# Performance work log

Hardware: AMD Instinct MI355X
Metric: run time of the kernel (lower is better)

The kernel has to match this reference:

```python
import jax, jax.numpy as jnp
import numpy as np

S, B, I, H, O = 1024, 64, 512, 2048, 512


def setup_inputs() -> dict:
    key = jax.random.key(0)
    k1, k2, k3, k4, k5 = jax.random.split(key, 5)
    X = jax.random.normal(k1, (S, B, I), dtype=jnp.float32)
    W_ih = jax.random.normal(k2, (H, I), dtype=jnp.float32) * (1.0 / np.sqrt(I))
    hh = jax.random.uniform(k3, (H,), dtype=jnp.float32)  # clamped-to-[-1,1] diagonal recurrence
    W_ho = jax.random.normal(k4, (O, H), dtype=jnp.float32) * (1.0 / np.sqrt(H))
    b_ho = jax.random.normal(k5, (O,), dtype=jnp.float32) * 0.01
    return {"X": X, "W_ih": W_ih, "hh": hh, "W_ho": W_ho, "b_ho": b_ho}


def reference(X, W_ih, hh, W_ho, b_ho):
    # Batch the input->hidden projection over the whole sequence in one GEMM:
    # u[s,b,h] = X[s,b,i] @ W_ih[h,i]^T
    u = jnp.einsum('sbi,hi->sbh', X, W_ih)
    h0 = jnp.zeros((X.shape[1], W_ih.shape[0]), dtype=X.dtype)

    def step(h, u_t):
        h_new = jnp.abs(u_t + hh * h)
        return h_new, None

    h_final, _ = jax.lax.scan(step, h0, u)
    Y = h_final @ W_ho.T + b_ho  # [B, O]
    return Y
```

## Files before the change

kernel.cpp:

```cpp
#include <hip/hip_runtime.h>
#include <hip/hip_bf16.h>
#include <stdint.h>

#define S_LEN 1024
#define B_SZ  64
#define I_SZ  512
#define H_SZ  2048
#define O_SZ  512
#define BH    (B_SZ * H_SZ)

typedef __bf16  bf16x8 __attribute__((ext_vector_type(8)));
typedef float   f32x4  __attribute__((ext_vector_type(4)));

static __device__ __forceinline__ ushort f2bf(float f) {
  union { float f; unsigned u; } v; v.f = f;
  unsigned r = v.u + 0x7FFFu + ((v.u >> 16) & 1u);
  return (ushort)(r >> 16);
}
static __device__ __forceinline__ float bf2f(ushort u) {
  return __builtin_bit_cast(float, (unsigned)u << 16);
}

#define GLOAD_LDS16(gp, lp) \
  __builtin_amdgcn_global_load_lds( \
      (__attribute__((address_space(1))) void*)(gp), \
      (__attribute__((address_space(3))) void*)(lp), 16, 0, 0)

__global__ __launch_bounds__(256) void convert_f32_bf16_kernel(
    const float4* __restrict__ in, ushort4* __restrict__ out, int n4) {
  int i = blockIdx.x * 256 + threadIdx.x;
  if (i >= n4) return;
  float4 v = in[i];
  ushort4 o; o.x = f2bf(v.x); o.y = f2bf(v.y); o.z = f2bf(v.z); o.w = f2bf(v.w);
  out[i] = o;
}

__global__ __launch_bounds__(256, 3) void fused_gemm_scan_kernel(
    const float* __restrict__ X,
    const ushort* __restrict__ Wbf,
    const float* __restrict__ hh,
    float* __restrict__ hstate) {
  __shared__ __align__(16) ushort smem[17408];
  ushort* As = smem;
  ushort* Bs = smem + 9216;
  ushort* Cs = smem;

  const int tid  = threadIdx.x;
  const int wave = tid >> 6;
  const int lane = tid & 63;

  const int bid = blockIdx.x;
  const int x = bid & 7;
  const int g = bid >> 3;
  const int b  = (x << 3) | (g & 7);
  const int ht = g >> 3;

  const int wm = (wave >> 1) * 64;
  const int wn = (wave & 1) * 64;
  const int ml = lane & 15;
  const int q  = lane >> 4;

  const int arow0 = wave * 32 + (lane >> 3);
  const size_t offA = (size_t)arow0 * (B_SZ * I_SZ) + (size_t)b * I_SZ + (lane & 7) * 8;

  const int r0     = wave * 32;
  const int srow   = lane >> 3;
  const int schunk = ((lane & 7) - srow) & 7;
  const ushort* gB = Wbf + (size_t)(ht * 128 + r0 + srow) * I_SZ + schunk * 8;
  ushort* lB = Bs + r0 * 64;

  int aoff[2], boff[2];
  aoff[0] = q * 8;
  aoff[1] = (4 + q) * 8;
  boff[0] = ((q + ml) & 7) * 8;
  boff[1] = ((4 + q + ml) & 7) * 8;
  int arow[4], brow[4];
  #pragma unroll
  for (int i = 0; i < 4; ++i) {
    arow[i] = (wm + i * 16 + ml) * 72;
    brow[i] = (wn + i * 16 + ml) * 64;
  }

  float c = 0.0f, p = 0.0f;
  if (tid < 128) c = hh[ht * 128 + tid];

  float4 ar[8];
  {
    const float* gp = X + offA;
    #pragma unroll
    for (int j = 0; j < 4; ++j) {
      ar[2 * j]     = *(const float4*)(gp + (size_t)j * (8 * B_SZ * I_SZ));
      ar[2 * j + 1] = *(const float4*)(gp + (size_t)j * (8 * B_SZ * I_SZ) + 4);
    }
  }

  for (int st = 0; st < 8; ++st) {
    f32x4 acc[4][4] = {};

    for (int kt = 0; kt < I_SZ / 64; ++kt) {
      __syncthreads();
      #pragma unroll
      for (int j = 0; j < 4; ++j) {
        union { __bf16 h[8]; uint4 v; } uvt;
        uvt.h[0] = (__bf16)ar[2 * j].x;     uvt.h[1] = (__bf16)ar[2 * j].y;
        uvt.h[2] = (__bf16)ar[2 * j].z;     uvt.h[3] = (__bf16)ar[2 * j].w;
        uvt.h[4] = (__bf16)ar[2 * j + 1].x; uvt.h[5] = (__bf16)ar[2 * j + 1].y;
        uvt.h[6] = (__bf16)ar[2 * j + 1].z; uvt.h[7] = (__bf16)ar[2 * j + 1].w;
        *(uint4*)&As[(arow0 + j * 8) * 72 + (lane & 7) * 8] = uvt.v;
      }
      #pragma unroll
      for (int jj = 0; jj < 4; ++jj)
        GLOAD_LDS16(gB + (size_t)(jj * 8) * I_SZ + kt * 64, lB + jj * 512);
      {
        int nst = (kt == 7) ? st + 1 : st;
        int nkt = (kt == 7) ? 0 : kt + 1;
        if (nst < 8) {
          const float* gp = X + offA + (size_t)nst * (128 * B_SZ * I_SZ) + nkt * 64;
          #pragma unroll
          for (int j = 0; j < 4; ++j) {
            ar[2 * j]     = *(const float4*)(gp + (size_t)j * (8 * B_SZ * I_SZ));
            ar[2 * j + 1] = *(const float4*)(gp + (size_t)j * (8 * B_SZ * I_SZ) + 4);
          }
        }
      }
      __syncthreads();
      #pragma unroll
      for (int ks = 0; ks < 2; ++ks) {
        bf16x8 af[4], bfr[4];
        #pragma unroll
        for (int i = 0; i < 4; ++i) {
          af[i]  = *(const bf16x8*)&As[arow[i] + (ks * 4) * 8 + aoff[0] - q * 8 + q * 8];
          bfr[i] = *(const bf16x8*)&Bs[brow[i] + boff[ks]];
        }
        #pragma unroll
        for (int i = 0; i < 4; ++i)
          af[i] = *(const bf16x8*)&As[arow[i] + (ks * 4 + q) * 8];
        #pragma unroll
        for (int mi = 0; mi < 4; ++mi)
          #pragma unroll
          for (int ni = 0; ni < 4; ++ni)
            acc[mi][ni] = __builtin_amdgcn_mfma_f32_16x16x32_bf16(
                af[mi], bfr[ni], acc[mi][ni], 0, 0, 0);
      }
    }

    __syncthreads();
    const int sb = wm + q * 4;
    #pragma unroll
    for (int mi = 0; mi < 4; ++mi) {
      #pragma unroll
      for (int ni = 0; ni < 4; ++ni) {
        ushort4 o;
        o.x = f2bf(acc[mi][ni][0]); o.y = f2bf(acc[mi][ni][1]);
        o.z = f2bf(acc[mi][ni][2]); o.w = f2bf(acc[mi][ni][3]);
        *(ushort4*)&Cs[(wn + ni * 16 + ml) * 132 + sb + mi * 16] = o;
      }
    }
    __syncthreads();

    if (tid < 128) {
      const ushort* col = &Cs[tid * 132];
      #pragma unroll
      for (int s0 = 0; s0 < 128; s0 += 16) {
        ushort4 v0 = *(const ushort4*)&col[s0];
        ushort4 v1 = *(const ushort4*)&col[s0 + 4];
        ushort4 v2 = *(const ushort4*)&col[s0 + 8];
        ushort4 v3 = *(const ushort4*)&col[s0 + 12];
        p = fmaf(c, fabsf(p), bf2f(v0.x)); p = fmaf(c, fabsf(p), bf2f(v0.y));
        p = fmaf(c, fabsf(p), bf2f(v0.z)); p = fmaf(c, fabsf(p), bf2f(v0.w));
        p = fmaf(c, fabsf(p), bf2f(v1.x)); p = fmaf(c, fabsf(p), bf2f(v1.y));
        p = fmaf(c, fabsf(p), bf2f(v1.z)); p = fmaf(c, fabsf(p), bf2f(v1.w));
        p = fmaf(c, fabsf(p), bf2f(v2.x)); p = fmaf(c, fabsf(p), bf2f(v2.y));
        p = fmaf(c, fabsf(p), bf2f(v2.z)); p = fmaf(c, fabsf(p), bf2f(v2.w));
        p = fmaf(c, fabsf(p), bf2f(v3.x)); p = fmaf(c, fabsf(p), bf2f(v3.y));
        p = fmaf(c, fabsf(p), bf2f(v3.z)); p = fmaf(c, fabsf(p), bf2f(v3.w));
      }
    }
  }

  if (tid < 128) hstate[(size_t)b * H_SZ + ht * 128 + tid] = fabsf(p);
}

__global__ __launch_bounds__(256) void init_y_kernel(
    const float* __restrict__ bho, float* __restrict__ Y) {
  int idx = blockIdx.x * 256 + threadIdx.x;
  Y[idx] = bho[idx & (O_SZ - 1)];
}

__global__ __launch_bounds__(256) void final_tiled_kernel(
    const float* __restrict__ hstate, const float* __restrict__ Who,
    float* __restrict__ Y) {
  __shared__ float Ws[64 * 68];
  __shared__ float Hs[64 * 68];
  const int tid = threadIdx.x;
  const int og = blockIdx.x, kc = blockIdx.y;
  const int to = tid & 15, tb = tid >> 4;
  float acc[4][4] = {};
  #pragma unroll
  for (int ks = 0; ks < 2; ++ks) {
    const int k0 = kc * 128 + ks * 64;
    const int r = tid >> 2, cg = (tid & 3) * 16;
    #pragma unroll
    for (int i2 = 0; i2 < 4; ++i2) {
      *(float4*)&Ws[r * 68 + cg + i2 * 4] =
          *(const float4*)&Who[(size_t)(og * 64 + r) * H_SZ + k0 + cg + i2 * 4];
      *(float4*)&Hs[r * 68 + cg + i2 * 4] =
          *(const float4*)&hstate[(size_t)r * H_SZ + k0 + cg + i2 * 4];
    }
    __syncthreads();
    #pragma unroll 4
    for (int k = 0; k < 64; ++k) {
      float wv[4], hv[4];
      #pragma unroll
      for (int jj2 = 0; jj2 < 4; ++jj2) wv[jj2] = Ws[(to * 4 + jj2) * 68 + k];
      #pragma unroll
      for (int ii = 0; ii < 4; ++ii) hv[ii] = Hs[(tb * 4 + ii) * 68 + k];
      #pragma unroll
      for (int ii = 0; ii < 4; ++ii)
        #pragma unroll
        for (int jj2 = 0; jj2 < 4; ++jj2)
          acc[ii][jj2] += hv[ii] * wv[jj2];
    }
    __syncthreads();
  }
  #pragma unroll
  for (int ii = 0; ii < 4; ++ii)
    #pragma unroll
    for (int jj2 = 0; jj2 < 4; ++jj2)
      atomicAdd(&Y[(size_t)(tb * 4 + ii) * O_SZ + og * 64 + to * 4 + jj2],
                acc[ii][jj2]);
}

extern "C" void kernel_launch(void* const* d_in, const int* in_sizes, int n_in,
                              void* d_out, int out_size, void* d_ws, size_t ws_size,
                              hipStream_t stream) {
  (void)in_sizes; (void)n_in; (void)out_size; (void)ws_size;
  const float* X   = (const float*)d_in[0];
  const float* Wih = (const float*)d_in[1];
  const float* hh  = (const float*)d_in[2];
  const float* Who = (const float*)d_in[3];
  const float* bho = (const float*)d_in[4];
  float* Y = (float*)d_out;

  const size_t WBF = (size_t)H_SZ * I_SZ * 2;

  char* w = (char*)d_ws;
  ushort* Wbf    = (ushort*)w;
  float*  hstate = (float*) (w + WBF);

  {
    int n4w = (int)((size_t)H_SZ * I_SZ / 4);
    convert_f32_bf16_kernel<<<n4w / 256, 256, 0, stream>>>(
        (const float4*)Wih, (ushort4*)Wbf, n4w);
  }

  fused_gemm_scan_kernel<<<1024, 256, 0, stream>>>(X, Wbf, hh, hstate);

  init_y_kernel<<<(B_SZ * O_SZ) / 256, 256, 0, stream>>>(bho, Y);
  final_tiled_kernel<<<dim3(O_SZ / 64, 16), 256, 0, stream>>>(hstate, Who, Y);
}
```

Measured before the change: 387.6 us.

## Software-pipeline fused GEMM-scan, overlap scan with next tile, fuse output projection

Restructures the fused GEMM+scan kernel into a single flattened loop over 64 k-steps. Global-to-LDS loads for the next step and the A conversion for the step after are issued before the current MFMAs, with explicit waitcnt and barrier control. The result tile now has its own LDS region, so the scan of the previous 128-step chunk runs in the same iterations as the next chunk's GEMM instead of serialising after it. The output projection is folded into the kernel's epilogue using atomics, removing the hstate round trip and the separate final kernel. The cost is doubled LDS, occupancy dropping from 3 to 2 blocks, and redundant Who reads across blocks.

Result: slower. 418.1 us (+7.9%).

```diff
diff --git a/kernel.cpp b/kernel.cpp
--- a/kernel.cpp
+++ b/kernel.cpp
@@ -7,7 +7,6 @@
 #define I_SZ  512
 #define H_SZ  2048
 #define O_SZ  512
-#define BH    (B_SZ * H_SZ)
 
 typedef __bf16  bf16x8 __attribute__((ext_vector_type(8)));
 typedef float   f32x4  __attribute__((ext_vector_type(4)));
@@ -35,25 +34,67 @@
   out[i] = o;
 }
 
-__global__ __launch_bounds__(256, 3) void fused_gemm_scan_kernel(
+__global__ __launch_bounds__(256) void init_y_kernel(
+    const float* __restrict__ bho, float* __restrict__ Y) {
+  int idx = blockIdx.x * 256 + threadIdx.x;
+  Y[idx] = bho[idx & (O_SZ - 1)];
+}
+
+#define CVT_WRITE_A() do { \
+    _Pragma("unroll") \
+    for (int j_ = 0; j_ < 4; ++j_) { \
+      union { __bf16 h[8]; uint4 v; } uvt_; \
+      uvt_.h[0] = (__bf16)ar[2*j_].x;   uvt_.h[1] = (__bf16)ar[2*j_].y; \
+      uvt_.h[2] = (__bf16)ar[2*j_].z;   uvt_.h[3] = (__bf16)ar[2*j_].w; \
+      uvt_.h[4] = (__bf16)ar[2*j_+1].x; uvt_.h[5] = (__bf16)ar[2*j_+1].y; \
+      uvt_.h[6] = (__bf16)ar[2*j_+1].z; uvt_.h[7] = (__bf16)ar[2*j_+1].w; \
+      *(uint4*)&As[(arow0 + j_ * 8) * 72 + (lane & 7) * 8] = uvt_.v; \
+    } } while (0)
+
+#define PREFETCH_A(T) do { \
+    const float* gp_ = X + offA + (size_t)((T) >> 3) * (128 * B_SZ * I_SZ) \
+                         + (size_t)(((T) & 7) * 64); \
+    _Pragma("unroll") \
+    for (int j_ = 0; j_ < 4; ++j_) { \
+      ar[2*j_]   = *(const float4*)(gp_ + (size_t)j_ * (8 * B_SZ * I_SZ)); \
+      ar[2*j_+1] = *(const float4*)(gp_ + (size_t)j_ * (8 * B_SZ * I_SZ) + 4); \
+    } } while (0)
+
+#define SCAN16(colp, s0_) do { \
+    ushort4 v0 = *(const ushort4*)&(colp)[(s0_)]; \
+    ushort4 v1 = *(const ushort4*)&(colp)[(s0_) + 4]; \
+    ushort4 v2 = *(const ushort4*)&(colp)[(s0_) + 8]; \
+    ushort4 v3 = *(const ushort4*)&(colp)[(s0_) + 12]; \
+    p = fmaf(c, fabsf(p), bf2f(v0.x)); p = fmaf(c, fabsf(p), bf2f(v0.y)); \
+    p = fmaf(c, fabsf(p), bf2f(v0.z)); p = fmaf(c, fabsf(p), bf2f(v0.w)); \
+    p = fmaf(c, fabsf(p), bf2f(v1.x)); p = fmaf(c, fabsf(p), bf2f(v1.y)); \
+    p = fmaf(c, fabsf(p), bf2f(v1.z)); p = fmaf(c, fabsf(p), bf2f(v1.w)); \
+    p = fmaf(c, fabsf(p), bf2f(v2.x)); p = fmaf(c, fabsf(p), bf2f(v2.y)); \
+    p = fmaf(c, fabsf(p), bf2f(v2.z)); p = fmaf(c, fabsf(p), bf2f(v2.w)); \
+    p = fmaf(c, fabsf(p), bf2f(v3.x)); p = fmaf(c, fabsf(p), bf2f(v3.y)); \
+    p = fmaf(c, fabsf(p), bf2f(v3.z)); p = fmaf(c, fabsf(p), bf2f(v3.w)); \
+  } while (0)
+
+__global__ __launch_bounds__(256, 2) void fused_gemm_scan_kernel(
     const float* __restrict__ X,
     const ushort* __restrict__ Wbf,
     const float* __restrict__ hh,
-    float* __restrict__ hstate) {
-  __shared__ __align__(16) ushort smem[17408];
+    const float* __restrict__ Who,
+    float* __restrict__ Y) {
+  __shared__ __align__(16) ushort smem[34304];
   ushort* As = smem;
   ushort* Bs = smem + 9216;
-  ushort* Cs = smem;
+  ushort* Cs = smem + 17408;
 
   const int tid  = threadIdx.x;
   const int wave = tid >> 6;
   const int lane = tid & 63;
 
   const int bid = blockIdx.x;
-  const int x = bid & 7;
-  const int g = bid >> 3;
-  const int b  = (x << 3) | (g & 7);
-  const int ht = g >> 3;
+  const int xcd = bid & 7;
+  const int g   = bid >> 3;
+  const int b   = (xcd << 3) | (g & 7);
+  const int ht  = g >> 3;
 
   const int wm = (wave >> 1) * 64;
   const int wn = (wave & 1) * 64;
@@ -61,7 +102,8 @@
   const int q  = lane >> 4;
 
   const int arow0 = wave * 32 + (lane >> 3);
-  const size_t offA = (size_t)arow0 * (B_SZ * I_SZ) + (size_t)b * I_SZ + (lane & 7) * 8;
+  const size_t offA = (size_t)arow0 * (B_SZ * I_SZ) + (size_t)b * I_SZ
+                    + (size_t)((lane & 7) * 8);
 
   const int r0     = wave * 32;
   const int srow   = lane >> 3;
@@ -69,11 +111,10 @@
   const ushort* gB = Wbf + (size_t)(ht * 128 + r0 + srow) * I_SZ + schunk * 8;
   ushort* lB = Bs + r0 * 64;
 
-  int aoff[2], boff[2];
-  aoff[0] = q * 8;
-  aoff[1] = (4 + q) * 8;
-  boff[0] = ((q + ml) & 7) * 8;
-  boff[1] = ((4 + q + ml) & 7) * 8;
+  const int aoff0 = q * 8;
+  const int aoff1 = (4 + q) * 8;
+  const int boff0 = ((q + ml) & 7) * 8;
+  const int boff1 = ((4 + q + ml) & 7) * 8;
   int arow[4], brow[4];
   #pragma unroll
   for (int i = 0; i < 4; ++i) {
@@ -85,150 +126,131 @@
   if (tid < 128) c = hh[ht * 128 + tid];
 
   float4 ar[8];
+
+  #pragma unroll
+  for (int jj = 0; jj < 4; ++jj)
+    GLOAD_LDS16(gB + (size_t)(jj * 8) * I_SZ, lB + jj * 512);
+  __builtin_amdgcn_sched_barrier(0);
+  PREFETCH_A(0);
+  CVT_WRITE_A();
+  PREFETCH_A(1);
+  __builtin_amdgcn_sched_barrier(0);
+  asm volatile("s_waitcnt vmcnt(8) lgkmcnt(0)" ::: "memory");
+  __builtin_amdgcn_sched_barrier(0);
+  __builtin_amdgcn_s_barrier();
+
+  f32x4 acc[4][4];
+
+  #pragma unroll 1
+  for (int t = 0; t < 64; ++t) {
+    const int kt = t & 7;
+    if (kt == 0) {
+      #pragma unroll
+      for (int mi = 0; mi < 4; ++mi)
+        #pragma unroll
+        for (int ni = 0; ni < 4; ++ni) {
+          f32x4 z = {0.f, 0.f, 0.f, 0.f};
+          acc[mi][ni] = z;
+        }
+    }
+
+    bf16x8 a0[4], a1[4], b0[4], b1[4];
+    #pragma unroll
+    for (int i = 0; i < 4; ++i) {
+      a0[i] = *(const bf16x8*)&As[arow[i] + aoff0];
+      a1[i] = *(const bf16x8*)&As[arow[i] + aoff1];
+      b0[i] = *(const bf16x8*)&Bs[brow[i] + boff0];
+      b1[i] = *(const bf16x8*)&Bs[brow[i] + boff1];
+    }
+    __builtin_amdgcn_sched_barrier(0);
+    asm volatile("s_waitcnt lgkmcnt(0)" ::: "memory");
+    __builtin_amdgcn_sched_barrier(0);
+    __builtin_amdgcn_s_barrier();
+
+    if (t < 63) {
+      const int k1 = (t + 1) & 7;
+      #pragma unroll
+      for (int jj = 0; jj < 4; ++jj)
+        GLOAD_LDS16(gB + (size_t)(jj * 8) * I_SZ + k1 * 64, lB + jj * 512);
+    }
+    __builtin_amdgcn_sched_barrier(0);
+    if (t < 63) {
+      CVT_WRITE_A();
+      if (t < 62) PREFETCH_A(t + 2);
+    }
+
+    if (t >= 8 && tid < 128) {
+      const ushort* col = &Cs[tid * 132];
+      const int s0 = kt * 16;
+      SCAN16(col, s0);
+    }
+
+    __builtin_amdgcn_s_setprio(1);
+    #pragma unroll
+    for (int mi = 0; mi < 4; ++mi)
+      #pragma unroll
+      for (int ni = 0; ni < 4; ++ni)
+        acc[mi][ni] = __builtin_amdgcn_mfma_f32_16x16x32_bf16(
+            a0[mi], b0[ni], acc[mi][ni], 0, 0, 0);
+    #pragma unroll
+    for (int mi = 0; mi < 4; ++mi)
+      #pragma unroll
+      for (int ni = 0; ni < 4; ++ni)
+        acc[mi][ni] = __builtin_amdgcn_mfma_f32_16x16x32_bf16(
+            a1[mi], b1[ni], acc[mi][ni], 0, 0, 0);
+    __builtin_amdgcn_s_setprio(0);
+
+    __builtin_amdgcn_sched_barrier(0);
+    if (t < 62) {
+      asm volatile("s_waitcnt vmcnt(8) lgkmcnt(0)" ::: "memory");
+    } else {
+      asm volatile("s_waitcnt vmcnt(0) lgkmcnt(0)" ::: "memory");
+    }
+    __builtin_amdgcn_sched_barrier(0);
+    __builtin_amdgcn_s_barrier();
+
+    if (kt == 7) {
+      const int sb = wm + q * 4;
+      #pragma unroll
+      for (int mi = 0; mi < 4; ++mi)
+        #pragma unroll
+        for (int ni = 0; ni < 4; ++ni) {
+          ushort4 o;
+          o.x = f2bf(acc[mi][ni][0]); o.y = f2bf(acc[mi][ni][1]);
+          o.z = f2bf(acc[mi][ni][2]); o.w = f2bf(acc[mi][ni][3]);
+          *(ushort4*)&Cs[(wn + ni * 16 + ml) * 132 + sb + mi * 16] = o;
+        }
+    }
+  }
+
+  __syncthreads();
+
+  if (tid < 128) {
+    const ushort* col = &Cs[tid * 132];
+    #pragma unroll
+    for (int s0 = 0; s0 < 128; s0 += 16) {
+      SCAN16(col, s0);
+    }
+    ((float*)smem)[tid] = fabsf(p);
+  }
+  __syncthreads();
+
   {
-    const float* gp = X + offA;
-    #pragma unroll
-    for (int j = 0; j < 4; ++j) {
-      ar[2 * j]     = *(const float4*)(gp + (size_t)j * (8 * B_SZ * I_SZ));
-      ar[2 * j + 1] = *(const float4*)(gp + (size_t)j * (8 * B_SZ * I_SZ) + 4);
-    }
-  }
-
-  for (int st = 0; st < 8; ++st) {
-    f32x4 acc[4][4] = {};
-
-    for (int kt = 0; kt < I_SZ / 64; ++kt) {
-      __syncthreads();
-      #pragma unroll
-      for (int j = 0; j < 4; ++j) {
-        union { __bf16 h[8]; uint4 v; } uvt;
-        uvt.h[0] = (__bf16)ar[2 * j].x;     uvt.h[1] = (__bf16)ar[2 * j].y;
-        uvt.h[2] = (__bf16)ar[2 * j].z;     uvt.h[3] = (__bf16)ar[2 * j].w;
-        uvt.h[4] = (__bf16)ar[2 * j + 1].x; uvt.h[5] = (__bf16)ar[2 * j + 1].y;
-        uvt.h[6] = (__bf16)ar[2 * j + 1].z; uvt.h[7] = (__bf16)ar[2 * j + 1].w;
-        *(uint4*)&As[(arow0 + j * 8) * 72 + (lane & 7) * 8] = uvt.v;
-      }
-      #pragma unroll
-      for (int jj = 0; jj < 4; ++jj)
-        GLOAD_LDS16(gB + (size_t)(jj * 8) * I_SZ + kt * 64, lB + jj * 512);
-      {
-        int nst = (kt == 7) ? st + 1 : st;
-        int nkt = (kt == 7) ? 0 : kt + 1;
-        if (nst < 8) {
-          const float* gp = X + offA + (size_t)nst * (128 * B_SZ * I_SZ) + nkt * 64;
-          #pragma unroll
-          for (int j = 0; j < 4; ++j) {
-            ar[2 * j]     = *(const float4*)(gp + (size_t)j * (8 * B_SZ * I_SZ));
-            ar[2 * j + 1] = *(const float4*)(gp + (size_t)j * (8 * B_SZ * I_SZ) + 4);
-          }
-        }
-      }
-      __syncthreads();
-      #pragma unroll
-      for (int ks = 0; ks < 2; ++ks) {
-        bf16x8 af[4], bfr[4];
-        #pragma unroll
-        for (int i = 0; i < 4; ++i) {
-          af[i]  = *(const bf16x8*)&As[arow[i] + (ks * 4) * 8 + aoff[0] - q * 8 + q * 8];
-          bfr[i] = *(const bf16x8*)&Bs[brow[i] + boff[ks]];
-        }
-        #pragma unroll
-        for (int i = 0; i < 4; ++i)
-          af[i] = *(const bf16x8*)&As[arow[i] + (ks * 4 + q) * 8];
-        #pragma unroll
-        for (int mi = 0; mi < 4; ++mi)
-          #pragma unroll
-          for (int ni = 0; ni < 4; ++ni)
-            acc[mi][ni] = __builtin_amdgcn_mfma_f32_16x16x32_bf16(
-                af[mi], bfr[ni], acc[mi][ni], 0, 0, 0);
-      }
-    }
-
-    __syncthreads();
-    const int sb = wm + q * 4;
-    #pragma unroll
-    for (int mi = 0; mi < 4; ++mi) {
-      #pragma unroll
-      for (int ni = 0; ni < 4; ++ni) {
-        ushort4 o;
-        o.x = f2bf(acc[mi][ni][0]); o.y = f2bf(acc[mi][ni][1]);
-        o.z = f2bf(acc[mi][ni][2]); o.w = f2bf(acc[mi][ni][3]);
-        *(ushort4*)&Cs[(wn + ni * 16 + ml) * 132 + sb + mi * 16] = o;
-      }
-    }
-    __syncthreads();
-
-    if (tid < 128) {
-      const ushort* col = &Cs[tid * 132];
-      #pragma unroll
-      for (int s0 = 0; s0 < 128; s0 += 16) {
-        ushort4 v0 = *(const ushort4*)&col[s0];
-        ushort4 v1 = *(const ushort4*)&col[s0 + 4];
-        ushort4 v2 = *(const ushort4*)&col[s0 + 8];
-        ushort4 v3 = *(const ushort4*)&col[s0 + 12];
-        p = fmaf(c, fabsf(p), bf2f(v0.x)); p = fmaf(c, fabsf(p), bf2f(v0.y));
-        p = fmaf(c, fabsf(p), bf2f(v0.z)); p = fmaf(c, fabsf(p), bf2f(v0.w));
-        p = fmaf(c, fabsf(p), bf2f(v1.x)); p = fmaf(c, fabsf(p), bf2f(v1.y));
-        p = fmaf(c, fabsf(p), bf2f(v1.z)); p = fmaf(c, fabsf(p), bf2f(v1.w));
-        p = fmaf(c, fabsf(p), bf2f(v2.x)); p = fmaf(c, fabsf(p), bf2f(v2.y));
-        p = fmaf(c, fabsf(p), bf2f(v2.z)); p = fmaf(c, fabsf(p), bf2f(v2.w));
-        p = fmaf(c, fabsf(p), bf2f(v3.x)); p = fmaf(c, fabsf(p), bf2f(v3.y));
-        p = fmaf(c, fabsf(p), bf2f(v3.z)); p = fmaf(c, fabsf(p), bf2f(v3.w));
-      }
-    }
-  }
-
-  if (tid < 128) hstate[(size_t)b * H_SZ + ht * 128 + tid] = fabsf(p);
-}
-
-__global__ __launch_bounds__(256) void init_y_kernel(
-    const float* __restrict__ bho, float* __restrict__ Y) {
-  int idx = blockIdx.x * 256 + threadIdx.x;
-  Y[idx] = bho[idx & (O_SZ - 1)];
-}
-
-__global__ __launch_bounds__(256) void final_tiled_kernel(
-    const float* __restrict__ hstate, const float* __restrict__ Who,
-    float* __restrict__ Y) {
-  __shared__ float Ws[64 * 68];
-  __shared__ float Hs[64 * 68];
-  const int tid = threadIdx.x;
-  const int og = blockIdx.x, kc = blockIdx.y;
-  const int to = tid & 15, tb = tid >> 4;
-  float acc[4][4] = {};
-  #pragma unroll
-  for (int ks = 0; ks < 2; ++ks) {
-    const int k0 = kc * 128 + ks * 64;
-    const int r = tid >> 2, cg = (tid & 3) * 16;
-    #pragma unroll
-    for (int i2 = 0; i2 < 4; ++i2) {
-      *(float4*)&Ws[r * 68 + cg + i2 * 4] =
-          *(const float4*)&Who[(size_t)(og * 64 + r) * H_SZ + k0 + cg + i2 * 4];
-      *(float4*)&Hs[r * 68 + cg + i2 * 4] =
-          *(const float4*)&hstate[(size_t)r * H_SZ + k0 + cg + i2 * 4];
-    }
-    __syncthreads();
-    #pragma unroll 4
-    for (int k = 0; k < 64; ++k) {
-      float wv[4], hv[4];
-      #pragma unroll
-      for (int jj2 = 0; jj2 < 4; ++jj2) wv[jj2] = Ws[(to * 4 + jj2) * 68 + k];
-      #pragma unroll
-      for (int ii = 0; ii < 4; ++ii) hv[ii] = Hs[(tb * 4 + ii) * 68 + k];
-      #pragma unroll
-      for (int ii = 0; ii < 4; ++ii)
-        #pragma unroll
-        for (int jj2 = 0; jj2 < 4; ++jj2)
-          acc[ii][jj2] += hv[ii] * wv[jj2];
-    }
-    __syncthreads();
-  }
-  #pragma unroll
-  for (int ii = 0; ii < 4; ++ii)
-    #pragma unroll
-    for (int jj2 = 0; jj2 < 4; ++jj2)
-      atomicAdd(&Y[(size_t)(tb * 4 + ii) * O_SZ + og * 64 + to * 4 + jj2],
-                acc[ii][jj2]);
+    const float* hs = (const float*)smem;
+    const float* w0 = Who + (size_t)tid * H_SZ + (size_t)ht * 128;
+    const float* w1 = w0 + (size_t)256 * H_SZ;
+    float y0 = 0.f, y1 = 0.f;
+    #pragma unroll 8
+    for (int k = 0; k < 128; k += 4) {
+      float4 hv = *(const float4*)&hs[k];
+      float4 u0 = *(const float4*)&w0[k];
+      float4 u1 = *(const float4*)&w1[k];
+      y0 += hv.x * u0.x + hv.y * u0.y + hv.z * u0.z + hv.w * u0.w;
+      y1 += hv.x * u1.x + hv.y * u1.y + hv.z * u1.z + hv.w * u1.w;
+    }
+    atomicAdd(&Y[(size_t)b * O_SZ + tid], y0);
+    atomicAdd(&Y[(size_t)b * O_SZ + 256 + tid], y1);
+  }
 }
 
 extern "C" void kernel_launch(void* const* d_in, const int* in_sizes, int n_in,
@@ -242,11 +264,7 @@
   const float* bho = (const float*)d_in[4];
   float* Y = (float*)d_out;
 
-  const size_t WBF = (size_t)H_SZ * I_SZ * 2;
-
-  char* w = (char*)d_ws;
-  ushort* Wbf    = (ushort*)w;
-  float*  hstate = (float*) (w + WBF);
+  ushort* Wbf = (ushort*)d_ws;
 
   {
     int n4w = (int)((size_t)H_SZ * I_SZ / 4);
@@ -254,8 +272,7 @@
         (const float4*)Wih, (ushort4*)Wbf, n4w);
   }
 
-  fused_gemm_scan_kernel<<<1024, 256, 0, stream>>>(X, Wbf, hh, hstate);
-
   init_y_kernel<<<(B_SZ * O_SZ) / 256, 256, 0, stream>>>(bho, Y);
-  final_tiled_kernel<<<dim3(O_SZ / 64, 16), 256, 0, stream>>>(hstate, Who, Y);
-}
+
+  fused_gemm_scan_kernel<<<1024, 256, 0, stream>>>(X, Wbf, hh, Who, Y);
+}
```
